# Kernel tuning notes

Hardware: AMD Instinct MI355X
Metric: run time of the kernel (lower is better)

Reference implementation:

```python
import jax, jax.numpy as jnp
import numpy as np

EPS = 1e-08
STRIDE = 1
KSIZE = 3

def setup_inputs() -> dict:
    key = jax.random.key(0)
    k1, k2, k3 = jax.random.split(key, 3)
    b, cin, cout, hw = 8, 512, 512, 64
    img = jax.random.normal(k1, (b, cin, hw, hw), dtype=jnp.float32)
    s = jax.random.normal(k2, (b, cin), dtype=jnp.float32)
    # xavier_normal init scale: sqrt(2/(fan_in+fan_out)), fan = c*k*k
    fan = cin * KSIZE * KSIZE
    std = np.sqrt(2.0 / (fan + cout * KSIZE * KSIZE)).astype(np.float32)
    weight = jax.random.normal(k3, (cout, cin, KSIZE, KSIZE), dtype=jnp.float32) * std
    return {"img": img, "s": s, "weight": weight}

def _modulated_weights(weight, s):
    # weight: [O,I,k,k], s: [B,I] -> [B,O,I,k,k]
    w = weight[None] * (s[:, None, :, None, None] + 1.0)
    d = jax.lax.rsqrt(jnp.sum(w * w, axis=(2, 3, 4), keepdims=True) + EPS)
    return w * d

def _conv_one(x, w, padding):
    # x: [I,H,W], w: [O,I,k,k] -> [O,H',W']
    out = jax.lax.conv_general_dilated(
        x[None], w, window_strides=(STRIDE, STRIDE),
        padding=((padding, padding), (padding, padding)),
        dimension_numbers=("NCHW", "OIHW", "NCHW"))
    return out[0]

def reference(img, s, weight):
    b, c, h, wdt = img.shape
    assert h == wdt
    padding = ((STRIDE - 1) * h - STRIDE + KSIZE) // 2
    ws = _modulated_weights(weight, s)           # [B,O,I,k,k]
    out = jax.vmap(lambda x, w: _conv_one(x, w, padding))(img, ws)
    return out
```

## Files before the change

kernel.cpp:

```cpp
#include <hip/hip_runtime.h>

typedef __attribute__((ext_vector_type(8))) short bf16x8;
typedef __attribute__((ext_vector_type(4))) float f32x4;
typedef __attribute__((ext_vector_type(8))) unsigned short u16x8;
typedef unsigned int u32;
typedef unsigned short u16;

#define CIN 512
#define CO  512
#define HH  64
#define WW  64
#define BB  8
#define HP  66
#define WPAD 68
#define HPW (HP*WPAD)
#define KK  4608

#define SIG_BYTES  (BB*CO*4)
#define WMOD_ELEMS ((size_t)BB*9*64*CO*8)
#define WMOD_BYTES (WMOD_ELEMS*2)
#define IMGT_ELEMS ((size_t)BB*64*HP*WPAD*8)
#define IMGT_BYTES (IMGT_ELEMS*2)
#define WS_NEED    ((size_t)SIG_BYTES + WMOD_BYTES + IMGT_BYTES)

__device__ __forceinline__ u16 f2bf(float f) {
  union { float f; u32 u; } v; v.f = f;
  u32 r = (v.u + 0x7FFFu + ((v.u >> 16) & 1u)) >> 16;
  return (u16)r;
}

__global__ void k_sigma(const float* __restrict__ weight, const float* __restrict__ s,
                        float* __restrict__ sigma) {
  int o = blockIdx.x;
  int tid = threadIdx.x;
  const float* wrow = weight + (size_t)o * KK;
  float acc[BB];
#pragma unroll
  for (int b = 0; b < BB; ++b) acc[b] = 0.f;
  for (int e = tid; e < KK; e += 256) {
    float w = wrow[e];
    float w2 = w * w;
    int i = e / 9;
#pragma unroll
    for (int b = 0; b < BB; ++b) {
      float m = s[b * CIN + i] + 1.0f;
      acc[b] += w2 * m * m;
    }
  }
#pragma unroll
  for (int b = 0; b < BB; ++b) {
#pragma unroll
    for (int off = 32; off >= 1; off >>= 1)
      acc[b] += __shfl_down(acc[b], off);
  }
  __shared__ float red[4][BB];
  int wv = tid >> 6, ln = tid & 63;
  if (ln == 0) {
#pragma unroll
    for (int b = 0; b < BB; ++b) red[wv][b] = acc[b];
  }
  __syncthreads();
  if (tid < BB) {
    float t = red[0][tid] + red[1][tid] + red[2][tid] + red[3][tid];
    sigma[tid * CO + o] = rsqrtf(t + 1e-8f);
  }
}

__global__ __launch_bounds__(256) void k_wmod(const float* __restrict__ weight,
                                              const float* __restrict__ s,
                                              const float* __restrict__ sigma,
                                              u16* __restrict__ wmod) {
  __shared__ float lw[16][577];
  int bid = blockIdx.x;
  int oc = bid & 31, ic = bid >> 5;
  int o0 = oc * 16;
  int tid = threadIdx.x;
  const float* wsrc = weight + (size_t)o0 * KK + ic * 576;
#pragma unroll
  for (int k = 0; k < 9; ++k) {
    int f4 = tid + k * 256;
    int row = f4 / 144;
    int col = f4 - row * 144;
    float4 v = *(const float4*)(wsrc + (size_t)row * KK + col * 4);
    lw[row][col*4+0]=v.x; lw[row][col*4+1]=v.y; lw[row][col*4+2]=v.z; lw[row][col*4+3]=v.w;
  }
  __syncthreads();
  int o_l = tid & 15, kg_l = (tid >> 4) & 7;
#pragma unroll
  for (int k = 0; k < 36; ++k) {
    int bt = k * 2 + (tid >> 7);
    int b = bt / 9;
    int t = bt - b * 9;
    int o = o0 + o_l;
    float sig = sigma[b * CO + o];
    u16x8 ov;
#pragma unroll
    for (int j = 0; j < 8; ++j) {
      int il = kg_l * 8 + j;
      float w = lw[o_l][il * 9 + t];
      float m = s[b * CIN + ic * 64 + il] + 1.0f;
      ov[j] = f2bf(w * m * sig);
    }
    *(u16x8*)(wmod + ((size_t)(bt * 64 + (ic * 8 + kg_l)) * CO + o) * 8) = ov;
  }
}

__global__ void k_pad(u16* __restrict__ imgt) {
  int gid = blockIdx.x * 256 + threadIdx.x;
  int grp = gid & 63;
  int pos = gid >> 6;
  int b = pos / 264;
  int pr = pos - b * 264;
  int yp, xp;
  if (pr < 136) { yp = (pr < 68) ? 0 : 65; xp = (pr < 68) ? pr : pr - 68; }
  else { int q = pr - 136; yp = 1 + (q >> 1); xp = (q & 1) ? 67 : 0; }
  u16x8 z = {0,0,0,0,0,0,0,0};
  *(u16x8*)(imgt + (((size_t)(b * 64 + grp) * HP + yp) * WPAD + xp) * 8) = z;
}

__global__ void k_imgt(const float* __restrict__ img, u16* __restrict__ imgt) {
  int bid = blockIdx.x;
  int ic = bid & 7;  int r = bid >> 3;
  int xc = r & 1;    r >>= 1;
  int y  = r & 63;   int b = r >> 6;
  int tid = threadIdx.x;
  __shared__ float lt[64][33];
  {
    int ii = tid >> 2, xq = tid & 3;
    const float* src = img + (((size_t)(b * CIN + ic * 64 + ii)) * HH + y) * WW + xc * 32 + xq * 8;
    float4 v0 = *(const float4*)src;
    float4 v1 = *(const float4*)(src + 4);
    int xb = xq * 8;
    lt[ii][xb+0]=v0.x; lt[ii][xb+1]=v0.y; lt[ii][xb+2]=v0.z; lt[ii][xb+3]=v0.w;
    lt[ii][xb+4]=v1.x; lt[ii][xb+5]=v1.y; lt[ii][xb+6]=v1.z; lt[ii][xb+7]=v1.w;
  }
  __syncthreads();
  int xl = tid >> 3, iq = tid & 7;
  u16x8 ov;
#pragma unroll
  for (int j = 0; j < 8; ++j) ov[j] = f2bf(lt[iq*8+j][xl]);
  size_t dst = (((size_t)(b * 64 + ic * 8 + iq) * HP + (y + 1)) * WPAD + (xc * 32 + xl + 1)) * 8;
  *(u16x8*)(imgt + dst) = ov;
}

__device__ __forceinline__ void async16(const u16* g, void* lds) {
  __builtin_amdgcn_global_load_lds((const __attribute__((address_space(1))) u32*)g,
                                   (__attribute__((address_space(3))) u32*)lds, 16, 0, 0);
}

__global__ __launch_bounds__(512, 2) void k_conv(const u16* __restrict__ wmod,
                                                 const u16* __restrict__ imgt,
                                                 float* __restrict__ out) {
  __shared__ alignas(16) u16 abuf[3][8192];
  int bid = blockIdx.x;
  int b  = bid >> 5;
  int ot = (bid >> 4) & 1;
  int pt = bid & 15;
  int y0 = pt * 4, obase = ot * 256;
  int tid = threadIdx.x;
  int wave = tid >> 6, lane = tid & 63;
  int wm = wave >> 2, wn = wave & 3;
  int col0 = lane & 15, kg = lane >> 4;

  int kgr0 = tid >> 8;
  int o_l  = tid & 255;
  const u16* awsrc0 = wmod + ((size_t)((b * 576 + kgr0    ) * 512) + obase + o_l) * 8;
  const u16* awsrc1 = wmod + ((size_t)((b * 576 + kgr0 + 2) * 512) + obase + o_l) * 8;

  const u16* pB = imgt + (((size_t)(b * 64 + kg) * HP + (y0 + wn)) * WPAD + col0) * 8;

  f32x4 zero = {0.f, 0.f, 0.f, 0.f};
  f32x4 acc[8][4];
#pragma unroll
  for (int i = 0; i < 8; ++i)
#pragma unroll
    for (int j = 0; j < 4; ++j) acc[i][j] = zero;

  bf16x8 bregE[4], bregO[4];

#define SLOT(m) ((m) % 3)
#define ICCX(m) (ii2 + ((m) >= 18 ? 2 : ((m) >= 9 ? 1 : 0)))
#define TX(m)   ((m) % 9)

#define STAGE_A(slot, icc, t) do { \
  int aoff_ = ((t) * 64 + (icc) * 4) * 4096; \
  async16(awsrc0 + aoff_, (void*)(abuf[slot] + (size_t)tid * 8)); \
  async16(awsrc1 + aoff_, (void*)(abuf[slot] + (size_t)(tid + 512) * 8)); \
} while (0)

#define BPF(dst, icc, t) do { \
  const u16* pb_ = pB + (size_t)(icc) * (4 * HPW * 8); \
  dst[0] = *(const bf16x8*)(pb_ + (((t)/3) * WPAD +  0 + ((t)%3)) * 8); \
  dst[1] = *(const bf16x8*)(pb_ + (((t)/3) * WPAD + 16 + ((t)%3)) * 8); \
  dst[2] = *(const bf16x8*)(pb_ + (((t)/3) * WPAD + 32 + ((t)%3)) * 8); \
  dst[3] = *(const bf16x8*)(pb_ + (((t)/3) * WPAD + 48 + ((t)%3)) * 8); \
} while (0)

#define COMPUTE(j, BR) do { \
  const u16* ab_ = abuf[SLOT(j)] + ((size_t)kg * 256 + wm * 128 + col0) * 8; \
  bf16x8 a_[8]; \
  _Pragma("unroll") \
  for (int am = 0; am < 8; ++am) a_[am] = *(const bf16x8*)(ab_ + am * 128); \
  __builtin_amdgcn_s_setprio(1); \
  _Pragma("unroll") \
  for (int am = 0; am < 8; ++am) { \
    acc[am][0] = __builtin_amdgcn_mfma_f32_16x16x32_bf16(a_[am], BR[0], acc[am][0], 0, 0, 0); \
    acc[am][1] = __builtin_amdgcn_mfma_f32_16x16x32_bf16(a_[am], BR[1], acc[am][1], 0, 0, 0); \
    acc[am][2] = __builtin_amdgcn_mfma_f32_16x16x32_bf16(a_[am], BR[2], acc[am][2], 0, 0, 0); \
    acc[am][3] = __builtin_amdgcn_mfma_f32_16x16x32_bf16(a_[am], BR[3], acc[am][3], 0, 0, 0); \
  } \
  __builtin_amdgcn_s_setprio(0); \
} while (0)

#define STEP(j, BR_CUR, BR_NXT) do { \
  if (ii < 7 || (j) + 1 < 18) BPF(BR_NXT, ICCX((j)+1), TX((j)+1)); \
  if (ii < 7 || (j) + 2 < 18) STAGE_A(SLOT((j)+2), ICCX((j)+2), TX((j)+2)); \
  COMPUTE(j, BR_CUR); \
  if (ii < 7 || (j) < 17) { \
    if ((j) == 16) { asm volatile("s_waitcnt vmcnt(4)" ::: "memory"); } \
    else           { asm volatile("s_waitcnt vmcnt(6)" ::: "memory"); } \
    __builtin_amdgcn_s_barrier(); \
    __builtin_amdgcn_sched_barrier(0); \
  } \
} while (0)

  {
    int ii2 = 0;
    STAGE_A(0, 0, 0);
    STAGE_A(1, 0, 1);
    BPF(bregE, 0, 0);
  }
  asm volatile("s_waitcnt vmcnt(6)" ::: "memory");
  __builtin_amdgcn_s_barrier();
  __builtin_amdgcn_sched_barrier(0);

  for (int ii = 0; ii < 8; ++ii) {
    const int ii2 = 2 * ii;
    STEP(0,  bregE, bregO);  STEP(1,  bregO, bregE);
    STEP(2,  bregE, bregO);  STEP(3,  bregO, bregE);
    STEP(4,  bregE, bregO);  STEP(5,  bregO, bregE);
    STEP(6,  bregE, bregO);  STEP(7,  bregO, bregE);
    STEP(8,  bregE, bregO);  STEP(9,  bregO, bregE);
    STEP(10, bregE, bregO);  STEP(11, bregO, bregE);
    STEP(12, bregE, bregO);  STEP(13, bregO, bregE);
    STEP(14, bregE, bregO);  STEP(15, bregO, bregE);
    STEP(16, bregE, bregO);  STEP(17, bregO, bregE);
  }
#undef STEP
#undef COMPUTE
#undef BPF
#undef STAGE_A
#undef SLOT
#undef ICCX
#undef TX

  int y = y0 + wn;
#pragma unroll
  for (int am = 0; am < 8; ++am) {
    int o = obase + wm * 128 + am * 16 + kg * 4;
#pragma unroll
    for (int an = 0; an < 4; ++an) {
      int x = an * 16 + col0;
      float* op = out + (((size_t)(b * CO + o)) * HH + y) * WW + x;
#pragma unroll
      for (int rg = 0; rg < 4; ++rg)
        op[(size_t)rg * HH * WW] = acc[am][an][rg];
    }
  }
}

__global__ void k_naive(const float* __restrict__ img, const float* __restrict__ s,
                        const float* __restrict__ weight, const float* __restrict__ sigma,
                        float* __restrict__ out) {
  int bid = blockIdx.x;
  int y = bid & 63; int r = bid >> 6; int o = r & 511; int b = r >> 9;
  int x = threadIdx.x;
  float sig = sigma[b * CO + o];
  float acc = 0.f;
  for (int i = 0; i < CIN; ++i) {
    float m = s[b * CIN + i] + 1.0f;
    const float* wp = weight + ((size_t)o * CIN + i) * 9;
    const float* ip = img + ((size_t)(b * CIN + i)) * HH * WW;
#pragma unroll
    for (int ky = 0; ky < 3; ++ky) {
      int yy = y + ky - 1;
      if (yy < 0 || yy > 63) continue;
#pragma unroll
      for (int kx = 0; kx < 3; ++kx) {
        int xx = x + kx - 1;
        float iv = (xx >= 0 && xx < 64) ? ip[yy * 64 + xx] : 0.f;
        acc += wp[ky * 3 + kx] * m * iv;
      }
    }
  }
  out[((size_t)(b * CO + o) * HH + y) * WW + x] = acc * sig;
}

extern "C" void kernel_launch(void* const* d_in, const int* in_sizes, int n_in,
                              void* d_out, int out_size, void* d_ws, size_t ws_size,
                              hipStream_t stream) {
  const float* img    = (const float*)d_in[0];
  const float* s      = (const float*)d_in[1];
  const float* weight = (const float*)d_in[2];
  float* out = (float*)d_out;
  char* ws = (char*)d_ws;
  float* sigma = (float*)ws;

  if (ws_size >= WS_NEED) {
    u16* wmod = (u16*)(ws + SIG_BYTES);
    u16* imgt = (u16*)(ws + SIG_BYTES + WMOD_BYTES);
    k_sigma<<<512, 256, 0, stream>>>(weight, s, sigma);
    k_wmod<<<256, 256, 0, stream>>>(weight, s, sigma, wmod);
    k_pad<<<528, 256, 0, stream>>>(imgt);
    k_imgt<<<8192, 256, 0, stream>>>(img, imgt);
    k_conv<<<256, 512, 0, stream>>>(wmod, imgt, out);
  } else {
    k_sigma<<<512, 256, 0, stream>>>(weight, s, sigma);
    k_naive<<<BB * CO * HH, 64, 0, stream>>>(img, s, weight, sigma, out);
  }
}
```

Baseline: 177.0 us.

## Stage weights in three-tap groups with double buffering and remap block order

Restructures the conv main loop so A (modulated weight) tiles are staged into LDS three taps at a time into a double buffer, replacing the per-tap triple-buffer ring. Barriers drop from one per tap to one per three-tap group, which cuts synchronisation overhead, and the prefetch depth grows. It also remaps block indices so consecutive blocks belong to different batches, which changes how work spreads across the hardware and caches. LDS use doubles, from 48KB to 96KB per block, which may limit the two-blocks-per-CU occupancy target. The vmcnt wait counts are hand-tuned and must match the number of outstanding loads.

```diff
diff --git a/kernel.cpp b/kernel.cpp
--- a/kernel.cpp
+++ b/kernel.cpp
@@ -151,8 +151,9 @@
 __global__ __launch_bounds__(512, 2) void k_conv(const u16* __restrict__ wmod,
                                                  const u16* __restrict__ imgt,
                                                  float* __restrict__ out) {
-  __shared__ alignas(16) u16 abuf[3][8192];
-  int bid = blockIdx.x;
+  __shared__ alignas(16) u16 abuf[2][3][8192];
+  int bid0 = blockIdx.x;
+  int bid  = (bid0 & 7) * 32 + (bid0 >> 3);
   int b  = bid >> 5;
   int ot = (bid >> 4) & 1;
   int pt = bid & 15;
@@ -162,10 +163,8 @@
   int wm = wave >> 2, wn = wave & 3;
   int col0 = lane & 15, kg = lane >> 4;
 
-  int kgr0 = tid >> 8;
-  int o_l  = tid & 255;
-  const u16* awsrc0 = wmod + ((size_t)((b * 576 + kgr0    ) * 512) + obase + o_l) * 8;
-  const u16* awsrc1 = wmod + ((size_t)((b * 576 + kgr0 + 2) * 512) + obase + o_l) * 8;
+  const u16* awsrc0 = wmod + (((size_t)(b * 576 + (tid >> 8))) * 512 + obase + (tid & 255)) * 8;
+  const u16* awsrc1 = awsrc0 + 2 * 512 * 8;
 
   const u16* pB = imgt + (((size_t)(b * 64 + kg) * HP + (y0 + wn)) * WPAD + col0) * 8;
 
@@ -178,26 +177,24 @@
 
   bf16x8 bregE[4], bregO[4];
 
-#define SLOT(m) ((m) % 3)
-#define ICCX(m) (ii2 + ((m) >= 18 ? 2 : ((m) >= 9 ? 1 : 0)))
-#define TX(m)   ((m) % 9)
-
-#define STAGE_A(slot, icc, t) do { \
-  int aoff_ = ((t) * 64 + (icc) * 4) * 4096; \
-  async16(awsrc0 + aoff_, (void*)(abuf[slot] + (size_t)tid * 8)); \
-  async16(awsrc1 + aoff_, (void*)(abuf[slot] + (size_t)(tid + 512) * 8)); \
+#define STAGE3(slot, iccv, rv) do { \
+  _Pragma("unroll") \
+  for (int c_ = 0; c_ < 3; ++c_) { \
+    int aoff_ = ((3 * (rv) + c_) * 64 + (iccv) * 4) * 4096; \
+    async16(awsrc0 + aoff_, (void*)(&abuf[slot][c_][0] + (size_t)tid * 8)); \
+    async16(awsrc1 + aoff_, (void*)(&abuf[slot][c_][0] + (size_t)(tid + 512) * 8)); \
+  } } while (0)
+
+#define BPF(dst, iccv, tv) do { \
+  const u16* pb_ = pB + (size_t)(iccv) * (4 * HPW * 8); \
+  dst[0] = *(const bf16x8*)(pb_ + (((tv)/3) * WPAD +  0 + ((tv)%3)) * 8); \
+  dst[1] = *(const bf16x8*)(pb_ + (((tv)/3) * WPAD + 16 + ((tv)%3)) * 8); \
+  dst[2] = *(const bf16x8*)(pb_ + (((tv)/3) * WPAD + 32 + ((tv)%3)) * 8); \
+  dst[3] = *(const bf16x8*)(pb_ + (((tv)/3) * WPAD + 48 + ((tv)%3)) * 8); \
 } while (0)
 
-#define BPF(dst, icc, t) do { \
-  const u16* pb_ = pB + (size_t)(icc) * (4 * HPW * 8); \
-  dst[0] = *(const bf16x8*)(pb_ + (((t)/3) * WPAD +  0 + ((t)%3)) * 8); \
-  dst[1] = *(const bf16x8*)(pb_ + (((t)/3) * WPAD + 16 + ((t)%3)) * 8); \
-  dst[2] = *(const bf16x8*)(pb_ + (((t)/3) * WPAD + 32 + ((t)%3)) * 8); \
-  dst[3] = *(const bf16x8*)(pb_ + (((t)/3) * WPAD + 48 + ((t)%3)) * 8); \
-} while (0)
-
-#define COMPUTE(j, BR) do { \
-  const u16* ab_ = abuf[SLOT(j)] + ((size_t)kg * 256 + wm * 128 + col0) * 8; \
+#define COMPUTE(slot, c_, BR) do { \
+  const u16* ab_ = &abuf[slot][c_][(kg * 256 + wm * 128 + col0) * 8]; \
   bf16x8 a_[8]; \
   _Pragma("unroll") \
   for (int am = 0; am < 8; ++am) a_[am] = *(const bf16x8*)(ab_ + am * 128); \
@@ -212,47 +209,41 @@
   __builtin_amdgcn_s_setprio(0); \
 } while (0)
 
-#define STEP(j, BR_CUR, BR_NXT) do { \
-  if (ii < 7 || (j) + 1 < 18) BPF(BR_NXT, ICCX((j)+1), TX((j)+1)); \
-  if (ii < 7 || (j) + 2 < 18) STAGE_A(SLOT((j)+2), ICCX((j)+2), TX((j)+2)); \
-  COMPUTE(j, BR_CUR); \
-  if (ii < 7 || (j) < 17) { \
-    if ((j) == 16) { asm volatile("s_waitcnt vmcnt(4)" ::: "memory"); } \
-    else           { asm volatile("s_waitcnt vmcnt(6)" ::: "memory"); } \
-    __builtin_amdgcn_s_barrier(); \
-    __builtin_amdgcn_sched_barrier(0); \
-  } \
+#define GROUP(g, B0, B1) do { \
+  if (ii < 7 || (g) < 5) STAGE3((((g) + 1) & 1), ii2 + ((g) + 1) / 3, ((g) + 1) % 3); \
+  BPF(B1, ii2 + (3 * (g) + 1) / 9, (3 * (g) + 1) % 9); \
+  COMPUTE(((g) & 1), 0, B0); \
+  BPF(B0, ii2 + (3 * (g) + 2) / 9, (3 * (g) + 2) % 9); \
+  COMPUTE(((g) & 1), 1, B1); \
+  if (ii < 7 || 3 * (g) + 3 < 18) BPF(B1, ii2 + (3 * (g) + 3) / 9, (3 * (g) + 3) % 9); \
+  COMPUTE(((g) & 1), 2, B0); \
+  asm volatile("s_waitcnt vmcnt(12)" ::: "memory"); \
+  __builtin_amdgcn_s_barrier(); \
+  __builtin_amdgcn_sched_barrier(0); \
 } while (0)
 
   {
-    int ii2 = 0;
-    STAGE_A(0, 0, 0);
-    STAGE_A(1, 0, 1);
+    const int ii2 = 0;
+    STAGE3(0, 0, 0);
     BPF(bregE, 0, 0);
   }
-  asm volatile("s_waitcnt vmcnt(6)" ::: "memory");
+  asm volatile("s_waitcnt vmcnt(4)" ::: "memory");
   __builtin_amdgcn_s_barrier();
   __builtin_amdgcn_sched_barrier(0);
 
   for (int ii = 0; ii < 8; ++ii) {
     const int ii2 = 2 * ii;
-    STEP(0,  bregE, bregO);  STEP(1,  bregO, bregE);
-    STEP(2,  bregE, bregO);  STEP(3,  bregO, bregE);
-    STEP(4,  bregE, bregO);  STEP(5,  bregO, bregE);
-    STEP(6,  bregE, bregO);  STEP(7,  bregO, bregE);
-    STEP(8,  bregE, bregO);  STEP(9,  bregO, bregE);
-    STEP(10, bregE, bregO);  STEP(11, bregO, bregE);
-    STEP(12, bregE, bregO);  STEP(13, bregO, bregE);
-    STEP(14, bregE, bregO);  STEP(15, bregO, bregE);
-    STEP(16, bregE, bregO);  STEP(17, bregO, bregE);
-  }
-#undef STEP
+    GROUP(0, bregE, bregO);
+    GROUP(1, bregO, bregE);
+    GROUP(2, bregE, bregO);
+    GROUP(3, bregO, bregE);
+    GROUP(4, bregE, bregO);
+    GROUP(5, bregO, bregE);
+  }
+#undef GROUP
 #undef COMPUTE
 #undef BPF
-#undef STAGE_A
-#undef SLOT
-#undef ICCX
-#undef TX
+#undef STAGE3
 
   int y = y0 + wn;
 #pragma unroll
```

Result: faster. 171.0 us (-3.4%).
